# Performance work log

Hardware: AMD Instinct MI355X
Metric: run time of the kernel (lower is better)

Reference implementation:

```python
import jax, jax.numpy as jnp
import numpy as np

DIM = 1024


def setup_inputs() -> dict:
    key = jax.random.key(0)
    kx, kq, kk, kv, kp = jax.random.split(key, 5)
    scale = 1.0 / np.sqrt(DIM)  # ~PyTorch Linear init scale
    return {
        "x": jax.random.normal(kx, (4, 4096, DIM), dtype=jnp.float32),
        "Wq": jax.random.normal(kq, (DIM, DIM), dtype=jnp.float32) * scale,
        "Wk": jax.random.normal(kk, (DIM, DIM), dtype=jnp.float32) * scale,
        "Wv": jax.random.normal(kv, (DIM, DIM), dtype=jnp.float32) * scale,
        "Wp": jax.random.normal(kp, (DIM, DIM), dtype=jnp.float32) * scale,
    }


def reference(x, Wq, Wk, Wv, Wp):
    # nn.Linear: y = x @ W^T (no bias)
    q = jnp.einsum("bsd,ed->bse", x, Wq)
    k = jnp.einsum("bsd,ed->bse", x, Wk)
    v = jnp.einsum("bsd,ed->bse", x, Wv)
    dim = x.shape[-1]
    # maxP 'readout' scaling: 1/dim (instead of 1/sqrt(dim))
    scores = jnp.einsum("bqd,bkd->bqk", q, k) / dim
    attn = jax.nn.softmax(scores, axis=-1)
    out = jnp.einsum("bqk,bkd->bqd", attn, v)
    return jnp.einsum("bsd,ed->bse", out, Wp)
```

## Files before the change

kernel.cpp:

```cpp
#include <hip/hip_runtime.h>

typedef unsigned short u16;
typedef __attribute__((ext_vector_type(8))) short bf16x8;
typedef __attribute__((ext_vector_type(4))) float f32x4;
typedef __attribute__((ext_vector_type(4))) unsigned short us4;
typedef __attribute__((ext_vector_type(8))) unsigned short us8;

__device__ __forceinline__ u16 f2us(float f) {
  union { float f; unsigned u; } a; a.f = f;
  unsigned u = a.u;
  u += 0x7fffu + ((u >> 16) & 1u);
  return (u16)(u >> 16);
}
__device__ __forceinline__ float us2f(u16 h) {
  union { unsigned u; float f; } a; a.u = ((unsigned)h) << 16;
  return a.f;
}

#define GLDS(g, l) __builtin_amdgcn_global_load_lds( \
    (const __attribute__((address_space(1))) void*)(g), \
    (__attribute__((address_space(3))) void*)(l), 16, 0, 0)

__global__ __launch_bounds__(256) void convert_all(
    const float* __restrict__ x, const float* __restrict__ Wq,
    const float* __restrict__ Wk, const float* __restrict__ Wv,
    const float* __restrict__ Wp, u16* __restrict__ xb, u16* __restrict__ wb) {
  const int bid = blockIdx.x;
  const float* src;
  u16* dst;
  int off;
  if (bid < 16384) {
    src = x; dst = xb; off = bid * 256 + threadIdx.x;
  } else {
    const int w = (bid - 16384) >> 10;
    const int lb = (bid - 16384) & 1023;
    src = (w == 0) ? Wq : (w == 1) ? Wk : (w == 2) ? Wv : Wp;
    dst = wb + (size_t)w * 1048576;
    off = lb * 256 + threadIdx.x;
  }
  f32x4 v = ((const f32x4*)src)[off];
  us4 o;
  o.x = f2us(v.x); o.y = f2us(v.y); o.z = f2us(v.z); o.w = f2us(v.w);
  ((us4*)dst)[off] = o;
}

#define MFMA_QUAD(QR, QC)                                                        \
  do {                                                                           \
    __builtin_amdgcn_s_setprio(1);                                               \
    _Pragma("unroll") for (int m = 0; m < 4; ++m)                                \
    _Pragma("unroll") for (int n = 0; n < 2; ++n)                                \
    _Pragma("unroll") for (int s = 0; s < 2; ++s)                                \
      acc[(QR)*4 + m][(QC)*2 + n] = __builtin_amdgcn_mfma_f32_16x16x32_bf16(     \
          af[(QR)*4 + m][s], bf[(QC)*2 + n][s], acc[(QR)*4 + m][(QC)*2 + n],     \
          0, 0, 0);                                                              \
    __builtin_amdgcn_s_setprio(0);                                               \
  } while (0)

#define STAGE_A(buf, h, kb)                                                  \
  do {                                                                       \
    const int su_ = (h) * 128 * lda + (kb);                                  \
    GLDS(Ap + aoff0 + su_, As + (buf) * 16384 + (h) * 8192 + ldst0);         \
    GLDS(Ap + aoff1 + su_, As + (buf) * 16384 + (h) * 8192 + ldst1);         \
  } while (0)

#define STAGE_B(buf, h, kb)                                                  \
  do {                                                                       \
    const int su_ = (h) * 128 * ldb + (kb);                                  \
    GLDS(Bp + boff0 + su_, Bs + (buf) * 16384 + (h) * 8192 + ldst0);         \
    GLDS(Bp + boff1 + su_, Bs + (buf) * 16384 + (h) * 8192 + ldst1);         \
  } while (0)

template <int EP>
__global__ __launch_bounds__(512, 2) void gemm256(
    const u16* __restrict__ A0, const u16* __restrict__ A1,
    const u16* __restrict__ A2, const u16* __restrict__ A3,
    const u16* __restrict__ B0, const u16* __restrict__ B1,
    const u16* __restrict__ B2, const u16* __restrict__ B3,
    void* C0, void* C1, void* C2, void* C3,
    int K, int lda, int ldb, int ldc, float scale,
    float* __restrict__ aux) {
  __shared__ u16 As[32768];
  __shared__ u16 Bs[32768];
  const int tid = threadIdx.x;
  const int lane = tid & 63;
  const int wid = tid >> 6;
  const int wm = wid >> 2;
  const int wn = wid & 3;
  const int z = blockIdx.z;
  const u16* A = (z == 0) ? A0 : (z == 1) ? A1 : (z == 2) ? A2 : A3;
  const u16* B = (z == 0) ? B0 : (z == 1) ? B1 : (z == 2) ? B2 : B3;
  void* C = (z == 0) ? C0 : (z == 1) ? C1 : (z == 2) ? C2 : C3;

  const int gx = gridDim.x;
  const int nwg = gx * (int)gridDim.y;
  const int orig = (int)blockIdx.y * gx + (int)blockIdx.x;
  const int swz = (orig & 7) * (nwg >> 3) + (orig >> 3);
  const long trow = (long)(swz / gx) * 256;
  const long tcol = (long)(swz % gx) * 256;

  const int srow = tid >> 3;
  const int sgrp = (tid & 7) ^ (srow & 7);
  const int aoff0 = srow * lda + sgrp * 8;
  const int aoff1 = aoff0 + (lda << 6);
  const int boff0 = srow * ldb + sgrp * 8;
  const int boff1 = boff0 + (ldb << 6);
  const int ldst0 = (tid & ~63) * 8;
  const int ldst1 = ldst0 + 4096;
  const u16* Ap = A + trow * lda;
  const u16* Bp = B + tcol * ldb;

  const int l15x64 = (lane & 15) * 64;
  const int cs0 = ((((lane >> 4) * 8)) ^ ((lane & 7) * 8)) + l15x64;
  const int cs1 = ((32 + ((lane >> 4) * 8)) ^ ((lane & 7) * 8)) + l15x64;

  f32x4 acc[8][4];
  f32x4 zero = {0.f, 0.f, 0.f, 0.f};
#pragma unroll
  for (int m = 0; m < 8; ++m)
#pragma unroll
    for (int n = 0; n < 4; ++n) acc[m][n] = zero;

  const int NT = K >> 6;
  const int kmask = K - 1;

  STAGE_A(0, 0, 0);
  STAGE_A(0, 1, 0);
  STAGE_B(0, 0, 0);
  STAGE_B(0, 1, 0);
  STAGE_A(1, 0, 64 & kmask);
  STAGE_A(1, 1, 64 & kmask);
  asm volatile("s_waitcnt vmcnt(4)" ::: "memory");
  __builtin_amdgcn_s_barrier();

  for (int t = 0; t < NT; ++t) {
    const int cur = t & 1, nxt = cur ^ 1;
    const int kb1 = ((t + 1) << 6) & kmask;
    const int kb2 = ((t + 2) << 6) & kmask;
    const u16* Acur = As + cur * 16384 + wm * 8192;
    const u16* Bcur = Bs + cur * 16384 + (wn >> 1) * 8192 + (wn & 1) * 4096;
    bf16x8 af[8][2], bf[4][2];

#pragma unroll
    for (int m = 0; m < 4; ++m) {
      af[m][0] = *(const bf16x8*)(Acur + m * 1024 + cs0);
      af[m][1] = *(const bf16x8*)(Acur + m * 1024 + cs1);
    }
#pragma unroll
    for (int n = 0; n < 2; ++n) {
      bf[n][0] = *(const bf16x8*)(Bcur + n * 1024 + cs0);
      bf[n][1] = *(const bf16x8*)(Bcur + n * 1024 + cs1);
    }
    STAGE_B(nxt, 0, kb1);
    __builtin_amdgcn_s_barrier();
    MFMA_QUAD(0, 0);

#pragma unroll
    for (int m = 0; m < 4; ++m) {
      af[4 + m][0] = *(const bf16x8*)(Acur + (4 + m) * 1024 + cs0);
      af[4 + m][1] = *(const bf16x8*)(Acur + (4 + m) * 1024 + cs1);
    }
    STAGE_B(nxt, 1, kb1);
    __builtin_amdgcn_s_barrier();
    MFMA_QUAD(1, 0);

#pragma unroll
    for (int n = 0; n < 2; ++n) {
      bf[2 + n][0] = *(const bf16x8*)(Bcur + (2 + n) * 1024 + cs0);
      bf[2 + n][1] = *(const bf16x8*)(Bcur + (2 + n) * 1024 + cs1);
    }
    __builtin_amdgcn_s_barrier();
    MFMA_QUAD(0, 1);

    STAGE_A(cur, 0, kb2);
    STAGE_A(cur, 1, kb2);
    __builtin_amdgcn_s_barrier();
    MFMA_QUAD(1, 1);
    asm volatile("s_waitcnt vmcnt(4)" ::: "memory");
  }

  asm volatile("s_waitcnt vmcnt(0)" ::: "memory");

  if (EP == 0 || (EP == 3 && z != 2)) {
    u16* Cb = (u16*)C;
#pragma unroll
    for (int m = 0; m < 8; ++m) {
      int gr = (int)trow + wm * 128 + m * 16 + ((lane >> 4) << 2);
#pragma unroll
      for (int n = 0; n < 4; ++n) {
        int gc = (int)tcol + wn * 64 + n * 16 + (lane & 15);
        f32x4 v = acc[m][n];
#pragma unroll
        for (int j = 0; j < 4; ++j) Cb[(size_t)(gr + j) * ldc + gc] = f2us(v[j] * scale);
      }
    }
  } else if (EP == 3) {
    u16* Ct = (u16*)C;
#pragma unroll
    for (int m = 0; m < 8; ++m) {
      int gr = (int)trow + wm * 128 + m * 16 + ((lane >> 4) << 2);
      int b = gr >> 12;
      int sl = gr & 4095;
      u16* base = Ct + ((size_t)b << 22) + sl;
#pragma unroll
      for (int n = 0; n < 4; ++n) {
        int gc = (int)tcol + wn * 64 + n * 16 + (lane & 15);
        f32x4 v = acc[m][n];
        us4 o;
        o.x = f2us(v[0] * scale); o.y = f2us(v[1] * scale);
        o.z = f2us(v[2] * scale); o.w = f2us(v[3] * scale);
        *(us4*)(base + (size_t)gc * 4096) = o;
      }
    }
  } else if (EP == 4) {
    u16* Cb = (u16*)C;
    float* ps = aux + ((size_t)z << 18) + ((size_t)(int)(tcol >> 6) + wn) * 4096;
#pragma unroll
    for (int m = 0; m < 8; ++m) {
      int gr = (int)trow + wm * 128 + m * 16 + ((lane >> 4) << 2);
      float rs0 = 0.f, rs1 = 0.f, rs2 = 0.f, rs3 = 0.f;
#pragma unroll
      for (int n = 0; n < 4; ++n) {
        int gc = (int)tcol + wn * 64 + n * 16 + (lane & 15);
        f32x4 v = acc[m][n];
        float e0 = __expf(v[0] * scale);
        float e1 = __expf(v[1] * scale);
        float e2 = __expf(v[2] * scale);
        float e3 = __expf(v[3] * scale);
        Cb[(size_t)(gr + 0) * ldc + gc] = f2us(e0);
        Cb[(size_t)(gr + 1) * ldc + gc] = f2us(e1);
        Cb[(size_t)(gr + 2) * ldc + gc] = f2us(e2);
        Cb[(size_t)(gr + 3) * ldc + gc] = f2us(e3);
        rs0 += e0; rs1 += e1; rs2 += e2; rs3 += e3;
      }
#pragma unroll
      for (int o = 1; o < 16; o <<= 1) {
        rs0 += __shfl_xor(rs0, o);
        rs1 += __shfl_xor(rs1, o);
        rs2 += __shfl_xor(rs2, o);
        rs3 += __shfl_xor(rs3, o);
      }
      if ((lane & 15) == 0) {
        f32x4 rv = {rs0, rs1, rs2, rs3};
        *(f32x4*)&ps[gr] = rv;
      }
    }
  } else if (EP == 5) {
    const float* rs = aux + z * 4096;
    u16* Cb = (u16*)C;
#pragma unroll
    for (int m = 0; m < 8; ++m) {
      int gr = (int)trow + wm * 128 + m * 16 + ((lane >> 4) << 2);
      f32x4 rv = *(const f32x4*)&rs[gr];
#pragma unroll
      for (int n = 0; n < 4; ++n) {
        int gc = (int)tcol + wn * 64 + n * 16 + (lane & 15);
        f32x4 v = acc[m][n];
#pragma unroll
        for (int j = 0; j < 4; ++j) Cb[(size_t)(gr + j) * ldc + gc] = f2us(v[j] * rv[j]);
      }
    }
  } else {
    float* Cf = (float*)C;
#pragma unroll
    for (int m = 0; m < 8; ++m) {
      int gr = (int)trow + wm * 128 + m * 16 + ((lane >> 4) << 2);
#pragma unroll
      for (int n = 0; n < 4; ++n) {
        int gc = (int)tcol + wn * 64 + n * 16 + (lane & 15);
        f32x4 v = acc[m][n];
#pragma unroll
        for (int j = 0; j < 4; ++j) Cf[(size_t)(gr + j) * ldc + gc] = v[j] * scale;
      }
    }
  }
}

__global__ __launch_bounds__(256) void rowsum_inv(const float* __restrict__ psum,
                                                  float* __restrict__ rsinv) {
  const int r = blockIdx.x * 256 + threadIdx.x;
  const int zz = r >> 12;
  const int rl = r & 4095;
  const float* p = psum + ((size_t)zz << 18) + rl;
  float s = 0.f;
#pragma unroll 8
  for (int q = 0; q < 64; ++q) s += p[q * 4096];
  rsinv[r] = 1.f / s;
}

extern "C" void kernel_launch(void* const* d_in, const int* in_sizes, int n_in,
                              void* d_out, int out_size, void* d_ws, size_t ws_size,
                              hipStream_t stream) {
  (void)in_sizes; (void)n_in; (void)out_size;
  const float* x  = (const float*)d_in[0];
  const float* Wq = (const float*)d_in[1];
  const float* Wk = (const float*)d_in[2];
  const float* Wv = (const float*)d_in[3];
  const float* Wp = (const float*)d_in[4];

  if (ws_size < 209715200) return;
  char* ws = (char*)d_ws;
  u16* xb  = (u16*)(ws);
  u16* wqb = (u16*)(ws + 33554432);
  u16* wkb = wqb + 1048576;
  u16* wvb = wkb + 1048576;
  u16* wpb = wvb + 1048576;
  u16* Qb  = (u16*)(ws + 41943040);
  u16* Kb  = (u16*)(ws + 75497472);
  u16* Vt  = (u16*)(ws + 109051904);
  u16* Ssp = (u16*)(ws + 142606336);
  u16* O   = (u16*)(ws + 176160768);

  u16* S0 = (u16*)d_out;
  u16* S1 = S0 + 16777216;
  u16* S2 = xb;
  u16* S3 = Ssp;
  float* psum  = (float*)O;
  float* rsinv = (float*)Qb;

  convert_all<<<20480, 256, 0, stream>>>(x, Wq, Wk, Wv, Wp, xb, wqb);

  gemm256<3><<<dim3(4, 64, 3), 512, 0, stream>>>(
      xb, xb, xb, xb, wqb, wkb, wvb, wvb, Qb, Kb, Vt, Vt,
      1024, 1024, 1024, 1024, 1.f, nullptr);

  const u16 *Q0 = Qb, *Q1 = Qb + 4194304, *Q2 = Qb + 8388608, *Q3 = Qb + 12582912;
  const u16 *K0 = Kb, *K1 = Kb + 4194304, *K2 = Kb + 8388608, *K3 = Kb + 12582912;
  gemm256<4><<<dim3(16, 16, 4), 512, 0, stream>>>(Q0, Q1, Q2, Q3, K0, K1, K2, K3,
                                                  S0, S1, S2, S3, 1024, 1024, 1024, 4096,
                                                  1.f / 1024.f, psum);

  rowsum_inv<<<64, 256, 0, stream>>>(psum, rsinv);

  const u16 *V0 = Vt, *V1 = Vt + 4194304, *V2 = Vt + 8388608, *V3 = Vt + 12582912;
  u16 *O0 = O, *O1 = O + 4194304, *O2 = O + 8388608, *O3 = O + 12582912;
  gemm256<5><<<dim3(4, 16, 4), 512, 0, stream>>>(S0, S1, S2, S3, V0, V1, V2, V3,
                                                 O0, O1, O2, O3, 4096, 4096, 4096, 1024,
                                                 1.f, rsinv);

  gemm256<2><<<dim3(4, 64, 1), 512, 0, stream>>>(O, O, O, O, wpb, wpb, wpb, wpb,
                                                 d_out, d_out, d_out, d_out,
                                                 1024, 1024, 1024, 1024, 1.f, nullptr);
}
```

Before: 413.2 us.

## Unroll GEMM main loop by two with full A/B prefetch and fenced LDS reads

Restructures the 256x256 GEMM main loop into a two-iteration unroll with fixed buffer pointers. Both A and B tiles for the next k-step are now prefetched two stages ahead, interleaved with MFMA quads, and the vmcnt wait is raised to 8. Explicit lgkmcnt(0) fences with sched_barrier are placed before each MFMA group, along with extra workgroup barriers. The goal is to hide global-load latency and to control the instruction schedule. The extra barriers and fences may serialize the LDS reads with the MFMAs and reduce overlap.

After: 451.0 us. 1.09x slower.

```diff
diff --git a/kernel.cpp b/kernel.cpp
--- a/kernel.cpp
+++ b/kernel.cpp
@@ -70,6 +70,12 @@
     GLDS(Bp + boff1 + su_, Bs + (buf) * 16384 + (h) * 8192 + ldst1);         \
   } while (0)
 
+#define LGKM0_FENCE()                                   \
+  do {                                                  \
+    asm volatile("s_waitcnt lgkmcnt(0)" ::: "memory");  \
+    __builtin_amdgcn_sched_barrier(0);                  \
+  } while (0)
+
 template <int EP>
 __global__ __launch_bounds__(512, 2) void gemm256(
     const u16* __restrict__ A0, const u16* __restrict__ A1,
@@ -129,53 +135,106 @@
   STAGE_B(0, 1, 0);
   STAGE_A(1, 0, 64 & kmask);
   STAGE_A(1, 1, 64 & kmask);
-  asm volatile("s_waitcnt vmcnt(4)" ::: "memory");
+  STAGE_B(1, 0, 64 & kmask);
+  STAGE_B(1, 1, 64 & kmask);
+  asm volatile("s_waitcnt vmcnt(8)" ::: "memory");
   __builtin_amdgcn_s_barrier();
 
-  for (int t = 0; t < NT; ++t) {
-    const int cur = t & 1, nxt = cur ^ 1;
-    const int kb1 = ((t + 1) << 6) & kmask;
+  const u16* A0c = As + wm * 8192;
+  const u16* B0c = Bs + (wn >> 1) * 8192 + (wn & 1) * 4096;
+  const u16* A1c = A0c + 16384;
+  const u16* B1c = B0c + 16384;
+
+  for (int t = 0; t < NT; t += 2) {
     const int kb2 = ((t + 2) << 6) & kmask;
-    const u16* Acur = As + cur * 16384 + wm * 8192;
-    const u16* Bcur = Bs + cur * 16384 + (wn >> 1) * 8192 + (wn & 1) * 4096;
+    const int kb3 = ((t + 3) << 6) & kmask;
     bf16x8 af[8][2], bf[4][2];
 
 #pragma unroll
     for (int m = 0; m < 4; ++m) {
-      af[m][0] = *(const bf16x8*)(Acur + m * 1024 + cs0);
-      af[m][1] = *(const bf16x8*)(Acur + m * 1024 + cs1);
+      af[m][0] = *(const bf16x8*)(A0c + m * 1024 + cs0);
+      af[m][1] = *(const bf16x8*)(A0c + m * 1024 + cs1);
     }
 #pragma unroll
     for (int n = 0; n < 2; ++n) {
-      bf[n][0] = *(const bf16x8*)(Bcur + n * 1024 + cs0);
-      bf[n][1] = *(const bf16x8*)(Bcur + n * 1024 + cs1);
-    }
-    STAGE_B(nxt, 0, kb1);
-    __builtin_amdgcn_s_barrier();
+      bf[n][0] = *(const bf16x8*)(B0c + n * 1024 + cs0);
+      bf[n][1] = *(const bf16x8*)(B0c + n * 1024 + cs1);
+    }
+    __builtin_amdgcn_s_barrier();
+    LGKM0_FENCE();
     MFMA_QUAD(0, 0);
+    __builtin_amdgcn_s_barrier();
 
 #pragma unroll
     for (int m = 0; m < 4; ++m) {
-      af[4 + m][0] = *(const bf16x8*)(Acur + (4 + m) * 1024 + cs0);
-      af[4 + m][1] = *(const bf16x8*)(Acur + (4 + m) * 1024 + cs1);
-    }
-    STAGE_B(nxt, 1, kb1);
-    __builtin_amdgcn_s_barrier();
+      af[4 + m][0] = *(const bf16x8*)(A0c + (4 + m) * 1024 + cs0);
+      af[4 + m][1] = *(const bf16x8*)(A0c + (4 + m) * 1024 + cs1);
+    }
+#pragma unroll
+    for (int n = 0; n < 2; ++n) {
+      bf[2 + n][0] = *(const bf16x8*)(B0c + (2 + n) * 1024 + cs0);
+      bf[2 + n][1] = *(const bf16x8*)(B0c + (2 + n) * 1024 + cs1);
+    }
+    __builtin_amdgcn_s_barrier();
+    LGKM0_FENCE();
     MFMA_QUAD(1, 0);
-
+    __builtin_amdgcn_s_barrier();
+
+    STAGE_A(0, 0, kb2);
+    STAGE_B(0, 0, kb2);
+    __builtin_amdgcn_s_barrier();
+    MFMA_QUAD(0, 1);
+    __builtin_amdgcn_s_barrier();
+
+    STAGE_A(0, 1, kb2);
+    STAGE_B(0, 1, kb2);
+    __builtin_amdgcn_s_barrier();
+    MFMA_QUAD(1, 1);
+    asm volatile("s_waitcnt vmcnt(8)" ::: "memory");
+    __builtin_amdgcn_s_barrier();
+
+#pragma unroll
+    for (int m = 0; m < 4; ++m) {
+      af[m][0] = *(const bf16x8*)(A1c + m * 1024 + cs0);
+      af[m][1] = *(const bf16x8*)(A1c + m * 1024 + cs1);
+    }
 #pragma unroll
     for (int n = 0; n < 2; ++n) {
-      bf[2 + n][0] = *(const bf16x8*)(Bcur + (2 + n) * 1024 + cs0);
-      bf[2 + n][1] = *(const bf16x8*)(Bcur + (2 + n) * 1024 + cs1);
-    }
+      bf[n][0] = *(const bf16x8*)(B1c + n * 1024 + cs0);
+      bf[n][1] = *(const bf16x8*)(B1c + n * 1024 + cs1);
+    }
+    __builtin_amdgcn_s_barrier();
+    LGKM0_FENCE();
+    MFMA_QUAD(0, 0);
+    __builtin_amdgcn_s_barrier();
+
+#pragma unroll
+    for (int m = 0; m < 4; ++m) {
+      af[4 + m][0] = *(const bf16x8*)(A1c + (4 + m) * 1024 + cs0);
+      af[4 + m][1] = *(const bf16x8*)(A1c + (4 + m) * 1024 + cs1);
+    }
+#pragma unroll
+    for (int n = 0; n < 2; ++n) {
+      bf[2 + n][0] = *(const bf16x8*)(B1c + (2 + n) * 1024 + cs0);
+      bf[2 + n][1] = *(const bf16x8*)(B1c + (2 + n) * 1024 + cs1);
+    }
+    __builtin_amdgcn_s_barrier();
+    LGKM0_FENCE();
+    MFMA_QUAD(1, 0);
+    __builtin_amdgcn_s_barrier();
+
+    STAGE_A(1, 0, kb3);
+    STAGE_B(1, 0, kb3);
     __builtin_amdgcn_s_barrier();
     MFMA_QUAD(0, 1);
-
-    STAGE_A(cur, 0, kb2);
-    STAGE_A(cur, 1, kb2);
+    __builtin_amdgcn_s_barrier();
+
+    STAGE_A(1, 1, kb3);
+    STAGE_B(1, 1, kb3);
     __builtin_amdgcn_s_barrier();
     MFMA_QUAD(1, 1);
-    asm volatile("s_waitcnt vmcnt(4)" ::: "memory");
+    asm volatile("s_waitcnt vmcnt(8)" ::: "memory");
+    __builtin_amdgcn_s_barrier();
   }
 
   asm volatile("s_waitcnt vmcnt(0)" ::: "memory");
```
